# Optimization experiments

Measured on AMD Instinct MI355X. Metric: run time of the kernel, lower is better.

## Reference

```python
import jax, jax.numpy as jnp
import numpy as np

N_WIRES = 8


def setup_inputs() -> dict:
    key = jax.random.key(0)
    k1, k2, k3 = jax.random.split(key, 3)
    B, S, E = 8, 1024, 64
    x = jax.random.normal(k1, (B, S, E), jnp.float32)
    theta = jax.random.normal(k2, (N_WIRES,), jnp.float32) * 0.1  # trainable RX angles (shared QLayer across heads)
    V_CAT = 16
    combine_w = jax.random.normal(k3, (E, V_CAT), jnp.float32) / jnp.sqrt(jnp.float32(V_CAT))
    combine_b = jnp.zeros((E,), jnp.float32)
    return {"x": x, "theta": theta, "combine_w": combine_w, "combine_b": combine_b}


def _cnot(state, c, t):
    # state: [N] + [2]*N_WIRES ; wire w lives on axis w+1
    ca, ta = c + 1, t + 1
    s0 = jax.lax.index_in_dim(state, 0, axis=ca, keepdims=False)
    s1 = jax.lax.index_in_dim(state, 1, axis=ca, keepdims=False)
    ta2 = ta - 1 if ta > ca else ta  # control axis was removed
    s1 = jnp.flip(s1, axis=ta2)      # flip target bit where control == 1
    return jnp.stack([s0, s1], axis=ca)


def _qlayer(angles, theta):
    # angles: [N, 8]. RX(x) then trainable RX(theta) on same wire == RX(x+theta).
    half = 0.5 * (angles + theta)
    amp0 = jnp.cos(half).astype(jnp.complex64)          # <0|RX|0>
    amp1 = (-1j) * jnp.sin(half).astype(jnp.complex64)  # <1|RX|0>
    N = angles.shape[0]
    # product state over 8 wires -> [N, 256]
    state = jnp.ones((N, 1), jnp.complex64)
    for w in range(N_WIRES):
        per = jnp.stack([amp0[:, w], amp1[:, w]], axis=-1)  # [N, 2]
        state = (state[:, :, None] * per[:, None, :]).reshape(N, -1)
    state = state.reshape((N,) + (2,) * N_WIRES)
    # CNOT chain 0->1, ..., 6->7, then ring closure 7->0
    for w in range(N_WIRES - 1):
        state = _cnot(state, w, w + 1)
    state = _cnot(state, N_WIRES - 1, 0)
    probs = state.real ** 2 + state.imag ** 2
    exps = []
    for w in range(N_WIRES):
        axes = tuple(ax for ax in range(1, N_WIRES + 1) if ax != w + 1)
        marg = probs.sum(axis=axes)  # [N, 2]
        exps.append(marg[:, 0] - marg[:, 1])  # <Z_w>
    return jnp.stack(exps, axis=-1)  # [N, 8]


def reference(x, theta, combine_w, combine_b):
    B, S, E = x.shape
    d_k = E // N_WIRES  # == 8 (encoder needs exactly 8 angles)
    heads = x.reshape(B, S, N_WIRES, d_k).transpose(0, 2, 1, 3)  # [B, H, S, 8]
    meas = _qlayer(heads.reshape(-1, d_k), theta).reshape(B, N_WIRES, S, N_WIRES)
    # torch.chunk(3, -1) on size 8 -> splits of 3, 3, 2
    q, k, v = meas[..., :3], meas[..., 3:6], meas[..., 6:]
    scores = jnp.einsum('bhsd,bhtd->bhst', q, k) / jnp.sqrt(jnp.float32(E))
    attn = jax.nn.softmax(scores, axis=-1)
    out = jnp.einsum('bhst,bhtd->bhsd', attn, v)          # [B, H, S, 2]
    out = out.transpose(0, 2, 1, 3).reshape(B, S, -1)     # [B, S, 16]
    return out @ combine_w.T + combine_b
```

## Files before the change

kernel.cpp:

```cpp
#include <hip/hip_runtime.h>
#include <hip/hip_fp16.h>

#define NB 8
#define NS 1024
#define NH 8
#define NMONO 56
#define MPART 512


constexpr int PRED[NMONO] = {
    0,
    0, 0, 0,
    1, 2, 3, 2, 3, 3,
    4, 5, 6, 7, 8, 9, 7, 8, 9, 9,
    10,11,12,13,14,15,16,17,18,19,16,17,18,19,19,
    20,21,22,23,24,25,26,27,28,29,30,31,32,33,34,30,31,32,33,34,34};
constexpr int VARI[NMONO] = {
    0,
    0, 1, 2,
    0, 0, 0, 1, 1, 2,
    0, 0, 0, 0, 0, 0, 1, 1, 1, 2,
    0, 0, 0, 0, 0, 0, 0, 0, 0, 0, 1, 1, 1, 1, 2,
    0, 0, 0, 0, 0, 0, 0, 0, 0, 0, 0, 0, 0, 0, 0, 1, 1, 1, 1, 1, 2};
#define F6 0.166666666666667f
#define F12 0.0833333333333333f
#define F24 0.0416666666666667f
#define F120 0.00833333333333333f
constexpr float COEF[NMONO] = {
    1.f,
    1.f, 1.f, 1.f,
    0.5f, 1.f, 1.f, 0.5f, 1.f, 0.5f,
    F6, 0.5f, 0.5f, 0.5f, 1.f, 0.5f, F6, 0.5f, 0.5f, F6,
    F24, F6, F6, 0.25f, 0.5f, 0.25f, F6, 0.5f, 0.5f, F6, F24, F6, 0.25f, F6, F24,
    F120, F24, F24, F12, F6, F12, F12, 0.25f, 0.25f, F12, F24, F6, 0.25f, F6, F24,
    F120, F24, F12, F12, F24, F120};

__global__ __launch_bounds__(192) void moments_kernel(
        const float* __restrict__ x, const float* __restrict__ theta,
        float* __restrict__ part) {
    __shared__ float red[3][64][57];

    const int tid = threadIdx.x;
    const int bh = blockIdx.x >> 3;
    const int qt = blockIdx.x & 7;
    const int b = bh >> 3, h = bh & 7;
    const int t0 = qt * 128;

    float th[8];
#pragma unroll
    for (int j = 0; j < 8; ++j) th[j] = theta[j];

    const int w = tid >> 6, l = tid & 63;

    float acc[NMONO];
#pragma unroll
    for (int i = 0; i < NMONO; ++i) acc[i] = 0.f;

#pragma unroll 1
    for (int j = 0; j < 2; ++j) {
        int t = t0 + l + 64 * j;
        const float4* xp = (const float4*)(x + ((size_t)(b * NS + t)) * 64 + h * 8);
        float4 lo = xp[0], hi = xp[1];
        float c0 = __cosf(lo.x + th[0]);
        float c1 = __cosf(lo.y + th[1]);
        float c2 = __cosf(lo.z + th[2]);
        float c3 = __cosf(lo.w + th[3]);
        float c4 = __cosf(hi.x + th[4]);
        float c5 = __cosf(hi.y + th[5]);
        float c6 = __cosf(hi.z + th[6]);
        float c7 = __cosf(hi.w + th[7]);
        float k0 = ((c0 * c1) * c2) * c3;
        float k1 = k0 * c4;
        float k2 = k1 * c5;
        float v0 = k2 * c6;
        float v1 = v0 * c7;
        float wch = (w == 0) ? 1.f : ((w == 1) ? v0 : v1);

        float mono[NMONO];
        mono[0] = wch;
        acc[0] += wch;
#pragma unroll
        for (int i = 1; i < NMONO; ++i) {
            float var = (VARI[i] == 0) ? k0 : ((VARI[i] == 1) ? k1 : k2);
            mono[i] = mono[PRED[i]] * var;
            acc[i] += mono[i];
        }
    }
#pragma unroll
    for (int i = 0; i < NMONO; ++i) red[w][l][i] = acc[i];
    __syncthreads();

    if (l < NMONO) {
        float s0 = 0.f, s1 = 0.f, s2 = 0.f, s3 = 0.f;
#pragma unroll
        for (int r = 0; r < 16; ++r) {
            s0 += red[w][4 * r + 0][l];
            s1 += red[w][4 * r + 1][l];
            s2 += red[w][4 * r + 2][l];
            s3 += red[w][4 * r + 3][l];
        }
        part[(size_t)blockIdx.x * 168 + w * 56 + l] = ((s0 + s1) + (s2 + s3)) * COEF[l];
    }
}

__global__ __launch_bounds__(256) void eval_proj_kernel(
        const float* __restrict__ x, const float* __restrict__ theta,
        const float* __restrict__ part, const float* __restrict__ W,
        const float* __restrict__ bias, float* __restrict__ out) {
    __shared__ __align__(16) float MhL[8 * 172];
    __shared__ float WtL[16 * 65];
    __shared__ float biasL[64];
    __shared__ float attL[16][17];

    const int tid = threadIdx.x;
    const int b = blockIdx.x >> 6;
    const int sc = blockIdx.x & 63;
    const int s0 = sc * 16;

    for (int e = tid; e < 8 * 168; e += 256) {
        int h = e / 168, idx = e - h * 168;
        const float* p = part + ((size_t)((b * 8 + h) * 8)) * 168 + idx;
        float s = ((p[0] + p[168]) + (p[336] + p[504]))
                + ((p[672] + p[840]) + (p[1008] + p[1176]));
        MhL[h * 172 + idx] = s;
    }
    for (int i = tid; i < 1024; i += 256) WtL[(i & 15) * 65 + (i >> 4)] = W[i];
    if (tid < 64) biasL[tid] = bias[tid];
    __syncthreads();

    if (tid < 128) {
        const int h = tid >> 4, sl = tid & 15;
        const int s = s0 + sl;
        float th[8];
#pragma unroll
        for (int j = 0; j < 8; ++j) th[j] = theta[j];
        const float4* xp = (const float4*)(x + ((size_t)(b * NS + s)) * 64 + h * 8);
        float4 lo = xp[0], hi = xp[1];
        float c0 = __cosf(lo.x + th[0]);
        float c1 = __cosf(lo.y + th[1]);
        float c2 = __cosf(lo.z + th[2]);
        float c3 = __cosf(lo.w + th[3]);
        float c4 = __cosf(hi.x + th[4]);
        float c5 = __cosf(hi.y + th[5]);
        float c6 = __cosf(hi.z + th[6]);
        float c7 = __cosf(hi.w + th[7]);
        float m1 = c0 * c1;
        float m2 = m1 * c2;
        float m0 = ((c1 * c2) * (c3 * c4)) * ((c5 * c6) * c7);
        float q0 = m0 * 0.125f, q1 = m1 * 0.125f, q2 = m2 * 0.125f;

        float mono[NMONO];
        mono[0] = 1.f;
#pragma unroll
        for (int i = 1; i < NMONO; ++i)
            mono[i] = mono[PRED[i]] * ((VARI[i] == 0) ? q0 : ((VARI[i] == 1) ? q1 : q2));

        const float4* MS = (const float4*)&MhL[h * 172];
        const float4* MA = (const float4*)&MhL[h * 172 + 56];
        const float4* MB = (const float4*)&MhL[h * 172 + 112];
        float aS = 0.f, aA = 0.f, aB = 0.f;
#pragma unroll
        for (int g = 0; g < 14; ++g) {
            float4 ms = MS[g], ma = MA[g], mb = MB[g];
            float p0 = mono[g * 4 + 0], p1 = mono[g * 4 + 1];
            float p2 = mono[g * 4 + 2], p3 = mono[g * 4 + 3];
            aS = fmaf(p0, ms.x, aS); aS = fmaf(p1, ms.y, aS);
            aS = fmaf(p2, ms.z, aS); aS = fmaf(p3, ms.w, aS);
            aA = fmaf(p0, ma.x, aA); aA = fmaf(p1, ma.y, aA);
            aA = fmaf(p2, ma.z, aA); aA = fmaf(p3, ma.w, aA);
            aB = fmaf(p0, mb.x, aB); aB = fmaf(p1, mb.y, aB);
            aB = fmaf(p2, mb.z, aB); aB = fmaf(p3, mb.w, aB);
        }
        float inv = 1.0f / aS;
        attL[sl][2 * h]     = aA * inv;
        attL[sl][2 * h + 1] = aB * inv;
    }
    __syncthreads();

    {
        const int e = tid & 63, rr = tid >> 6;
#pragma unroll
        for (int j = 0; j < 4; ++j) {
            int row = rr * 4 + j;
            float acc = biasL[e];
#pragma unroll
            for (int jj = 0; jj < 16; ++jj)
                acc = fmaf(attL[row][jj], WtL[jj * 65 + e], acc);
            out[((size_t)(b * NS + s0 + row)) * 64 + e] = acc;
        }
    }
}

#define NPAD 1028
#define SPB 32
__global__ __launch_bounds__(256) void fused_kernel(const float* __restrict__ x,
                                                    const float* __restrict__ theta,
                                                    const float* __restrict__ W,
                                                    const float* __restrict__ bias,
                                                    float* __restrict__ out) {
    __shared__ __half2 kvA[NH][NPAD];
    __shared__ __half2 kvB[NH][NPAD];
    __shared__ __half  kvC[NH][NPAD];
    __shared__ float   attl[SPB][17];
    __shared__ float   Wt[16][64];
    __shared__ float   bl[64];

    const int tid = threadIdx.x;
    const int b = blockIdx.x >> 5;
    const int chunk = blockIdx.x & 31;

    float th[8];
#pragma unroll
    for (int j = 0; j < 8; ++j) th[j] = theta[j];

    for (int i = tid; i < 1024; i += 256) Wt[i & 15][i >> 4] = W[i];
    if (tid < 64) bl[tid] = bias[tid];

    for (int i = 0; i < 32; ++i) {
        int r = tid + (i << 8);
        int h = r & 7, t = r >> 3;
        const float4* xp = (const float4*)(x + (((size_t)(b * NS + t)) << 6) + h * 8);
        float4 lo = xp[0], hi = xp[1];
        float c0 = __cosf(lo.x + th[0]);
        float c1 = __cosf(lo.y + th[1]);
        float c2 = __cosf(lo.z + th[2]);
        float c3 = __cosf(lo.w + th[3]);
        float c4 = __cosf(hi.x + th[4]);
        float c5 = __cosf(hi.y + th[5]);
        float c6 = __cosf(hi.z + th[6]);
        float c7 = __cosf(hi.w + th[7]);
        float m3 = ((c0 * c1) * c2) * c3;
        float m4 = m3 * c4;
        float m5 = m4 * c5;
        float m6 = m5 * c6;
        float m7 = m6 * c7;
        kvA[h][t] = __floats2half2_rn(m3, m4);
        kvB[h][t] = __floats2half2_rn(m5, m6);
        kvC[h][t] = __float2half_rn(m7);
    }
    __syncthreads();

    {
        const int h = tid >> 5;
        const int sl = tid & 31;
        const int sg = chunk * SPB + sl;
        const float4* xp = (const float4*)(x + (((size_t)(b * NS + sg)) << 6) + h * 8);
        float4 lo = xp[0], hi = xp[1];
        float c0 = __cosf(lo.x + th[0]);
        float c1 = __cosf(lo.y + th[1]);
        float c2 = __cosf(lo.z + th[2]);
        float c3 = __cosf(lo.w + th[3]);
        float c4 = __cosf(hi.x + th[4]);
        float c5 = __cosf(hi.y + th[5]);
        float c6 = __cosf(hi.z + th[6]);
        float c7 = __cosf(hi.w + th[7]);
        float m1 = c0 * c1;
        float m2 = m1 * c2;
        float m0 = ((c1 * c2) * (c3 * c4)) * ((c5 * c6) * c7);
        float q0 = m0 * 0.125f, q1 = m1 * 0.125f, q2 = m2 * 0.125f;

        float sum = 0.f, a0 = 0.f, a1 = 0.f;
#pragma unroll 4
        for (int t = 0; t < NS; ++t) {
            float2 kk = __half22float2(kvA[h][t]);
            float2 kv = __half22float2(kvB[h][t]);
            float v1 = __half2float(kvC[h][t]);
            float sc = q0 * kk.x + q1 * kk.y + q2 * kv.x;
            float e = __expf(sc);
            sum += e;
            a0 += e * kv.y;
            a1 += e * v1;
        }
        float inv = 1.0f / sum;
        attl[sl][h * 2] = a0 * inv;
        attl[sl][h * 2 + 1] = a1 * inv;
    }
    __syncthreads();

    {
        const int e = tid & 63;
        const int rr = tid >> 6;
#pragma unroll
        for (int i = 0; i < 8; ++i) {
            int sl = rr * 8 + i;
            float acc = bl[e];
#pragma unroll
            for (int j = 0; j < 16; ++j)
                acc += attl[sl][j] * Wt[j][e];
            int sg = chunk * SPB + sl;
            out[(((size_t)(b * NS + sg)) << 6) + e] = acc;
        }
    }
}

extern "C" void kernel_launch(void* const* d_in, const int* in_sizes, int n_in,
                              void* d_out, int out_size, void* d_ws, size_t ws_size,
                              hipStream_t stream) {
    const float* x     = (const float*)d_in[0];
    const float* theta = (const float*)d_in[1];
    const float* W     = (const float*)d_in[2];
    const float* bias  = (const float*)d_in[3];
    float* out = (float*)d_out;

    if (ws_size >= (size_t)MPART * 168 * sizeof(float)) {
        float* part = (float*)d_ws;
        moments_kernel<<<dim3(MPART), dim3(192), 0, stream>>>(x, theta, part);
        eval_proj_kernel<<<dim3(512), dim3(256), 0, stream>>>(x, theta, part, W, bias, out);
    } else {
        fused_kernel<<<dim3(NB * (NS / SPB)), dim3(256), 0, stream>>>(x, theta, W, bias, out);
    }
}
```

Measured before the change: 69.27 us.

## Fuse moment accumulation and evaluation into a single kernel per batch chunk

Replaces the two-kernel pipeline (partial moment sums written to workspace, then evaluation plus projection) with one kernel. Each block recomputes the full per-head Taylor moment sums for its batch over all 1024 tokens, reduces them in shared memory, then evaluates attention and the output projection for 32 query rows. This removes the second launch and the workspace round trip. In exchange, every block of a batch repeats the same moment work, each thread carries three 56-entry accumulator arrays, and the larger shared-memory footprint may lower occupancy.

```diff
diff --git a/kernel.cpp b/kernel.cpp
--- a/kernel.cpp
+++ b/kernel.cpp
@@ -1,11 +1,9 @@
 #include <hip/hip_runtime.h>
-#include <hip/hip_fp16.h>
 
 #define NB 8
 #define NS 1024
 #define NH 8
 #define NMONO 56
-#define MPART 512
 
 
 constexpr int PRED[NMONO] = {
@@ -35,105 +33,108 @@
     F120, F24, F24, F12, F6, F12, F12, 0.25f, 0.25f, F12, F24, F6, 0.25f, F6, F24,
     F120, F24, F12, F12, F24, F120};
 
-__global__ __launch_bounds__(192) void moments_kernel(
+__global__ __launch_bounds__(256) void mhaq_kernel(
         const float* __restrict__ x, const float* __restrict__ theta,
-        float* __restrict__ part) {
-    __shared__ float red[3][64][57];
-
-    const int tid = threadIdx.x;
-    const int bh = blockIdx.x >> 3;
-    const int qt = blockIdx.x & 7;
-    const int b = bh >> 3, h = bh & 7;
-    const int t0 = qt * 128;
-
-    float th[8];
-#pragma unroll
-    for (int j = 0; j < 8; ++j) th[j] = theta[j];
-
-    const int w = tid >> 6, l = tid & 63;
-
-    float acc[NMONO];
-#pragma unroll
-    for (int i = 0; i < NMONO; ++i) acc[i] = 0.f;
-
-#pragma unroll 1
-    for (int j = 0; j < 2; ++j) {
-        int t = t0 + l + 64 * j;
-        const float4* xp = (const float4*)(x + ((size_t)(b * NS + t)) * 64 + h * 8);
-        float4 lo = xp[0], hi = xp[1];
-        float c0 = __cosf(lo.x + th[0]);
-        float c1 = __cosf(lo.y + th[1]);
-        float c2 = __cosf(lo.z + th[2]);
-        float c3 = __cosf(lo.w + th[3]);
-        float c4 = __cosf(hi.x + th[4]);
-        float c5 = __cosf(hi.y + th[5]);
-        float c6 = __cosf(hi.z + th[6]);
-        float c7 = __cosf(hi.w + th[7]);
-        float k0 = ((c0 * c1) * c2) * c3;
-        float k1 = k0 * c4;
-        float k2 = k1 * c5;
-        float v0 = k2 * c6;
-        float v1 = v0 * c7;
-        float wch = (w == 0) ? 1.f : ((w == 1) ? v0 : v1);
-
-        float mono[NMONO];
-        mono[0] = wch;
-        acc[0] += wch;
-#pragma unroll
-        for (int i = 1; i < NMONO; ++i) {
-            float var = (VARI[i] == 0) ? k0 : ((VARI[i] == 1) ? k1 : k2);
-            mono[i] = mono[PRED[i]] * var;
-            acc[i] += mono[i];
-        }
-    }
-#pragma unroll
-    for (int i = 0; i < NMONO; ++i) red[w][l][i] = acc[i];
-    __syncthreads();
-
-    if (l < NMONO) {
-        float s0 = 0.f, s1 = 0.f, s2 = 0.f, s3 = 0.f;
-#pragma unroll
-        for (int r = 0; r < 16; ++r) {
-            s0 += red[w][4 * r + 0][l];
-            s1 += red[w][4 * r + 1][l];
-            s2 += red[w][4 * r + 2][l];
-            s3 += red[w][4 * r + 3][l];
-        }
-        part[(size_t)blockIdx.x * 168 + w * 56 + l] = ((s0 + s1) + (s2 + s3)) * COEF[l];
-    }
-}
-
-__global__ __launch_bounds__(256) void eval_proj_kernel(
-        const float* __restrict__ x, const float* __restrict__ theta,
-        const float* __restrict__ part, const float* __restrict__ W,
-        const float* __restrict__ bias, float* __restrict__ out) {
-    __shared__ __align__(16) float MhL[8 * 172];
+        const float* __restrict__ W, const float* __restrict__ bias,
+        float* __restrict__ out) {
+    __shared__ float red[4][64][73];
+    __shared__ __align__(16) float Mh[8][176];
     __shared__ float WtL[16 * 65];
     __shared__ float biasL[64];
-    __shared__ float attL[16][17];
+    __shared__ float attL[32][17];
 
     const int tid = threadIdx.x;
-    const int b = blockIdx.x >> 6;
-    const int sc = blockIdx.x & 63;
-    const int s0 = sc * 16;
-
-    for (int e = tid; e < 8 * 168; e += 256) {
-        int h = e / 168, idx = e - h * 168;
-        const float* p = part + ((size_t)((b * 8 + h) * 8)) * 168 + idx;
-        float s = ((p[0] + p[168]) + (p[336] + p[504]))
-                + ((p[672] + p[840]) + (p[1008] + p[1176]));
-        MhL[h * 172 + idx] = s;
+    const int b = blockIdx.x >> 5;
+    const int sc = blockIdx.x & 31;
+    const int s0 = sc * 32;
+
+    for (int i = tid; i < 1024; i += 256)
+        WtL[(i & 15) * 65 + (i >> 4)] = W[i];
+    if (tid < 64) biasL[tid] = bias[tid];
+
+    float th[8];
+#pragma unroll
+    for (int j = 0; j < 8; ++j) th[j] = theta[j];
+
+    const int w = tid >> 6, l = tid & 63;
+
+#pragma unroll 1
+    for (int hh = 0; hh < 2; ++hh) {
+        const int h = 2 * w + hh;
+
+        float acc1[NMONO], accA[NMONO], accB[NMONO];
+#pragma unroll
+        for (int i = 0; i < NMONO; ++i) { acc1[i] = 0.f; accA[i] = 0.f; accB[i] = 0.f; }
+
+#pragma unroll 1
+        for (int step = 0; step < 16; ++step) {
+            int t = step * 64 + l;
+            const float4* xp = (const float4*)(x + ((size_t)(b * NS + t)) * 64 + h * 8);
+            float4 lo = xp[0], hi = xp[1];
+            float c0 = __cosf(lo.x + th[0]);
+            float c1 = __cosf(lo.y + th[1]);
+            float c2 = __cosf(lo.z + th[2]);
+            float c3 = __cosf(lo.w + th[3]);
+            float c4 = __cosf(hi.x + th[4]);
+            float c5 = __cosf(hi.y + th[5]);
+            float c6 = __cosf(hi.z + th[6]);
+            float c7 = __cosf(hi.w + th[7]);
+            float k0 = ((c0 * c1) * c2) * c3;
+            float k1 = k0 * c4;
+            float k2 = k1 * c5;
+            float v0 = k2 * c6;
+            float v1 = v0 * c7;
+
+            float mono[NMONO];
+            mono[0] = 1.f;
+            acc1[0] += 1.f;
+            accA[0] += v0;
+            accB[0] += v1;
+#pragma unroll
+            for (int i = 1; i < NMONO; ++i) {
+                float var = (VARI[i] == 0) ? k0 : ((VARI[i] == 1) ? k1 : k2);
+                mono[i] = mono[PRED[i]] * var;
+                acc1[i] += mono[i];
+                accA[i] = fmaf(mono[i], v0, accA[i]);
+                accB[i] = fmaf(mono[i], v1, accB[i]);
+            }
+        }
+
+#pragma unroll
+        for (int i = 0; i < NMONO; ++i) red[w][l][i] = acc1[i];
+        __syncthreads();
+        if (l < NMONO) {
+            float s = 0.f;
+#pragma unroll
+            for (int r = 0; r < 64; ++r) s += red[w][r][l];
+            Mh[h][l] = s * COEF[l];
+        }
+        __syncthreads();
+#pragma unroll
+        for (int i = 0; i < NMONO; ++i) red[w][l][i] = accA[i];
+        __syncthreads();
+        if (l < NMONO) {
+            float s = 0.f;
+#pragma unroll
+            for (int r = 0; r < 64; ++r) s += red[w][r][l];
+            Mh[h][56 + l] = s * COEF[l];
+        }
+        __syncthreads();
+#pragma unroll
+        for (int i = 0; i < NMONO; ++i) red[w][l][i] = accB[i];
+        __syncthreads();
+        if (l < NMONO) {
+            float s = 0.f;
+#pragma unroll
+            for (int r = 0; r < 64; ++r) s += red[w][r][l];
+            Mh[h][112 + l] = s * COEF[l];
+        }
+        __syncthreads();
     }
-    for (int i = tid; i < 1024; i += 256) WtL[(i & 15) * 65 + (i >> 4)] = W[i];
-    if (tid < 64) biasL[tid] = bias[tid];
-    __syncthreads();
-
-    if (tid < 128) {
-        const int h = tid >> 4, sl = tid & 15;
+
+    {
+        const int h = tid >> 5, sl = tid & 31;
         const int s = s0 + sl;
-        float th[8];
-#pragma unroll
-        for (int j = 0; j < 8; ++j) th[j] = theta[j];
         const float4* xp = (const float4*)(x + ((size_t)(b * NS + s)) * 64 + h * 8);
         float4 lo = xp[0], hi = xp[1];
         float c0 = __cosf(lo.x + th[0]);
@@ -155,9 +156,9 @@
         for (int i = 1; i < NMONO; ++i)
             mono[i] = mono[PRED[i]] * ((VARI[i] == 0) ? q0 : ((VARI[i] == 1) ? q1 : q2));
 
-        const float4* MS = (const float4*)&MhL[h * 172];
-        const float4* MA = (const float4*)&MhL[h * 172 + 56];
-        const float4* MB = (const float4*)&MhL[h * 172 + 112];
+        const float4* MS = (const float4*)&Mh[h][0];
+        const float4* MA = (const float4*)&Mh[h][56];
+        const float4* MB = (const float4*)&Mh[h][112];
         float aS = 0.f, aA = 0.f, aB = 0.f;
 #pragma unroll
         for (int g = 0; g < 14; ++g) {
@@ -180,115 +181,13 @@
     {
         const int e = tid & 63, rr = tid >> 6;
 #pragma unroll
-        for (int j = 0; j < 4; ++j) {
-            int row = rr * 4 + j;
+        for (int j = 0; j < 8; ++j) {
+            int row = rr * 8 + j;
             float acc = biasL[e];
 #pragma unroll
             for (int jj = 0; jj < 16; ++jj)
                 acc = fmaf(attL[row][jj], WtL[jj * 65 + e], acc);
             out[((size_t)(b * NS + s0 + row)) * 64 + e] = acc;
-        }
-    }
-}
-
-#define NPAD 1028
-#define SPB 32
-__global__ __launch_bounds__(256) void fused_kernel(const float* __restrict__ x,
-                                                    const float* __restrict__ theta,
-                                                    const float* __restrict__ W,
-                                                    const float* __restrict__ bias,
-                                                    float* __restrict__ out) {
-    __shared__ __half2 kvA[NH][NPAD];
-    __shared__ __half2 kvB[NH][NPAD];
-    __shared__ __half  kvC[NH][NPAD];
-    __shared__ float   attl[SPB][17];
-    __shared__ float   Wt[16][64];
-    __shared__ float   bl[64];
-
-    const int tid = threadIdx.x;
-    const int b = blockIdx.x >> 5;
-    const int chunk = blockIdx.x & 31;
-
-    float th[8];
-#pragma unroll
-    for (int j = 0; j < 8; ++j) th[j] = theta[j];
-
-    for (int i = tid; i < 1024; i += 256) Wt[i & 15][i >> 4] = W[i];
-    if (tid < 64) bl[tid] = bias[tid];
-
-    for (int i = 0; i < 32; ++i) {
-        int r = tid + (i << 8);
-        int h = r & 7, t = r >> 3;
-        const float4* xp = (const float4*)(x + (((size_t)(b * NS + t)) << 6) + h * 8);
-        float4 lo = xp[0], hi = xp[1];
-        float c0 = __cosf(lo.x + th[0]);
-        float c1 = __cosf(lo.y + th[1]);
-        float c2 = __cosf(lo.z + th[2]);
-        float c3 = __cosf(lo.w + th[3]);
-        float c4 = __cosf(hi.x + th[4]);
-        float c5 = __cosf(hi.y + th[5]);
-        float c6 = __cosf(hi.z + th[6]);
-        float c7 = __cosf(hi.w + th[7]);
-        float m3 = ((c0 * c1) * c2) * c3;
-        float m4 = m3 * c4;
-        float m5 = m4 * c5;
-        float m6 = m5 * c6;
-        float m7 = m6 * c7;
-        kvA[h][t] = __floats2half2_rn(m3, m4);
-        kvB[h][t] = __floats2half2_rn(m5, m6);
-        kvC[h][t] = __float2half_rn(m7);
-    }
-    __syncthreads();
-
-    {
-        const int h = tid >> 5;
-        const int sl = tid & 31;
-        const int sg = chunk * SPB + sl;
-        const float4* xp = (const float4*)(x + (((size_t)(b * NS + sg)) << 6) + h * 8);
-        float4 lo = xp[0], hi = xp[1];
-        float c0 = __cosf(lo.x + th[0]);
-        float c1 = __cosf(lo.y + th[1]);
-        float c2 = __cosf(lo.z + th[2]);
-        float c3 = __cosf(lo.w + th[3]);
-        float c4 = __cosf(hi.x + th[4]);
-        float c5 = __cosf(hi.y + th[5]);
-        float c6 = __cosf(hi.z + th[6]);
-        float c7 = __cosf(hi.w + th[7]);
-        float m1 = c0 * c1;
-        float m2 = m1 * c2;
-        float m0 = ((c1 * c2) * (c3 * c4)) * ((c5 * c6) * c7);
-        float q0 = m0 * 0.125f, q1 = m1 * 0.125f, q2 = m2 * 0.125f;
-
-        float sum = 0.f, a0 = 0.f, a1 = 0.f;
-#pragma unroll 4
-        for (int t = 0; t < NS; ++t) {
-            float2 kk = __half22float2(kvA[h][t]);
-            float2 kv = __half22float2(kvB[h][t]);
-            float v1 = __half2float(kvC[h][t]);
-            float sc = q0 * kk.x + q1 * kk.y + q2 * kv.x;
-            float e = __expf(sc);
-            sum += e;
-            a0 += e * kv.y;
-            a1 += e * v1;
-        }
-        float inv = 1.0f / sum;
-        attl[sl][h * 2] = a0 * inv;
-        attl[sl][h * 2 + 1] = a1 * inv;
-    }
-    __syncthreads();
-
-    {
-        const int e = tid & 63;
-        const int rr = tid >> 6;
-#pragma unroll
-        for (int i = 0; i < 8; ++i) {
-            int sl = rr * 8 + i;
-            float acc = bl[e];
-#pragma unroll
-            for (int j = 0; j < 16; ++j)
-                acc += attl[sl][j] * Wt[j][e];
-            int sg = chunk * SPB + sl;
-            out[(((size_t)(b * NS + sg)) << 6) + e] = acc;
         }
     }
 }
@@ -302,11 +201,6 @@
     const float* bias  = (const float*)d_in[3];
     float* out = (float*)d_out;
 
-    if (ws_size >= (size_t)MPART * 168 * sizeof(float)) {
-        float* part = (float*)d_ws;
-        moments_kernel<<<dim3(MPART), dim3(192), 0, stream>>>(x, theta, part);
-        eval_proj_kernel<<<dim3(512), dim3(256), 0, stream>>>(x, theta, part, W, bias, out);
-    } else {
-        fused_kernel<<<dim3(NB * (NS / SPB)), dim3(256), 0, stream>>>(x, theta, W, bias, out);
-    }
+    (void)d_ws; (void)ws_size;
+    mhaq_kernel<<<dim3(NB * 32), dim3(256), 0, stream>>>(x, theta, W, bias, out);
 }
```

Result: slower. 88.69 us (+28.0%).
